# Optimization experiments

Hardware: AMD Instinct MI355X
Metric: run time of the kernel (lower is better)

The kernel has to match this reference:

```python
import jax, jax.numpy as jnp
import numpy as np

B, T, C, H = 4, 2048, 1024, 16
D = C // H  # head dim = 64


def _layernorm(x, g, b, eps=1e-5):
    mu = jnp.mean(x, axis=-1, keepdims=True)
    var = jnp.var(x, axis=-1, keepdims=True)
    return (x - mu) * jax.lax.rsqrt(var + eps) * g + b


def setup_inputs() -> dict:
    key = jax.random.key(0)
    ks = jax.random.split(key, 8)
    s = 0.02
    return {
        "x": jax.random.normal(ks[0], (B, T, C), dtype=jnp.float32),
        "ln1_g": jnp.ones((C,), jnp.float32),
        "ln1_b": jnp.zeros((C,), jnp.float32),
        "W_qkv": jax.random.normal(ks[1], (C, 3 * C), dtype=jnp.float32) * s,
        "b_qkv": jnp.zeros((3 * C,), jnp.float32),
        "W_o": jax.random.normal(ks[2], (C, C), dtype=jnp.float32) * s,
        "b_o": jnp.zeros((C,), jnp.float32),
        "ln2_g": jnp.ones((C,), jnp.float32),
        "ln2_b": jnp.zeros((C,), jnp.float32),
        "W_fc": jax.random.normal(ks[3], (C, 4 * C), dtype=jnp.float32) * s,
        "b_fc": jnp.zeros((4 * C,), jnp.float32),
        "W_pr": jax.random.normal(ks[4], (4 * C, C), dtype=jnp.float32) * s,
        "b_pr": jnp.zeros((C,), jnp.float32),
    }


def reference(x, ln1_g, ln1_b, W_qkv, b_qkv, W_o, b_o, ln2_g, ln2_b, W_fc, b_fc, W_pr, b_pr):
    # --- attention sub-block ---
    h = _layernorm(x, ln1_g, ln1_b)
    qkv = h @ W_qkv + b_qkv                       # [B,T,3C]
    q, k, v = jnp.split(qkv, 3, axis=-1)
    q = q.reshape(B, T, H, D).transpose(0, 2, 1, 3)  # [B,H,T,D]
    k = k.reshape(B, T, H, D).transpose(0, 2, 1, 3)
    v = v.reshape(B, T, H, D).transpose(0, 2, 1, 3)
    att = jnp.einsum("bhqd,bhkd->bhqk", q, k) * (1.0 / jnp.sqrt(jnp.float32(D)))
    causal = jnp.tril(jnp.ones((T, T), dtype=bool))
    att = jnp.where(causal, att, jnp.float32(-jnp.inf))
    att = jax.nn.softmax(att, axis=-1)
    y = jnp.einsum("bhqk,bhkd->bhqd", att, v)     # [B,H,T,D]
    y = y.transpose(0, 2, 1, 3).reshape(B, T, C)
    y = y @ W_o + b_o
    x = x + y
    # --- FFN sub-block ---
    h2 = _layernorm(x, ln2_g, ln2_b)
    f = jax.nn.gelu(h2 @ W_fc + b_fc, approximate=False)  # nn.GELU default = exact
    f = f @ W_pr + b_pr
    return x + f
```

## Files before the change

### kernel.cpp

```cpp
#include <hip/hip_runtime.h>
#include <math.h>

#define Bz 4
#define Tz 2048
#define Cz 1024
#define Hz 16
#define Dz 64
#define MTOK (Bz*Tz)

typedef __attribute__((ext_vector_type(8))) short short8;
typedef __attribute__((ext_vector_type(4))) short short4v;
typedef __attribute__((ext_vector_type(4))) float f32x4;

typedef unsigned int u32_g __attribute__((address_space(1)));
typedef unsigned int u32_l __attribute__((address_space(3)));

__device__ __forceinline__ unsigned short f2bf(float f) {
    unsigned int u = __float_as_uint(f);
    u += 0x7fffu + ((u >> 16) & 1u);
    return (unsigned short)(u >> 16);
}
__device__ __forceinline__ float bf2f(unsigned short h) {
    return __uint_as_float((unsigned int)h << 16);
}

__device__ __forceinline__ void async_cp16(const unsigned short* g, unsigned short* l) {
    __builtin_amdgcn_global_load_lds((const u32_g*)g, (u32_l*)l, 16, 0, 0);
}

__global__ void transpose_w(const float* __restrict__ W, unsigned short* __restrict__ Wt,
                            int K, int N) {
    __shared__ float tile[32][33];
    int n0 = blockIdx.x * 32, k0 = blockIdx.y * 32;
    int tx = threadIdx.x, ty = threadIdx.y;
    #pragma unroll
    for (int i = 0; i < 4; i++)
        tile[ty + i * 8][tx] = W[(size_t)(k0 + ty + i * 8) * N + n0 + tx];
    __syncthreads();
    #pragma unroll
    for (int i = 0; i < 4; i++)
        Wt[(size_t)(n0 + ty + i * 8) * K + k0 + tx] = f2bf(tile[tx][ty + i * 8]);
}

__global__ void ln_kernel(const float* __restrict__ x, const float* __restrict__ g,
                          const float* __restrict__ bb, unsigned short* __restrict__ out) {
    int tok = blockIdx.x, tid = threadIdx.x;
    const float4 v = ((const float4*)(x + (size_t)tok * Cz))[tid];
    float s = v.x + v.y + v.z + v.w;
    float sq = v.x * v.x + v.y * v.y + v.z * v.z + v.w * v.w;
    #pragma unroll
    for (int m = 1; m < 64; m <<= 1) { s += __shfl_xor(s, m); sq += __shfl_xor(sq, m); }
    __shared__ float red[8];
    int lane = tid & 63, wid = tid >> 6;
    if (!lane) { red[wid] = s; red[4 + wid] = sq; }
    __syncthreads();
    s = red[0] + red[1] + red[2] + red[3];
    sq = red[4] + red[5] + red[6] + red[7];
    float mu = s * (1.0f / Cz);
    float var = sq * (1.0f / Cz) - mu * mu;
    float rs = rsqrtf(var + 1e-5f);
    float4 gv = ((const float4*)g)[tid];
    float4 bv = ((const float4*)bb)[tid];
    short4v o;
    o[0] = f2bf((v.x - mu) * rs * gv.x + bv.x);
    o[1] = f2bf((v.y - mu) * rs * gv.y + bv.y);
    o[2] = f2bf((v.z - mu) * rs * gv.z + bv.z);
    o[3] = f2bf((v.w - mu) * rs * gv.w + bv.w);
    *(short4v*)(out + (size_t)tok * Cz + tid * 4) = o;
}

#define MODE_QKV 0
#define MODE_RESID 1
#define MODE_GELU 2

template <int MODE>
__launch_bounds__(256)
__global__ void gemm_bt(const unsigned short* __restrict__ A, const unsigned short* __restrict__ Bt,
                        int ld, int K, int N, const float* __restrict__ bias,
                        float* __restrict__ outf, unsigned short* __restrict__ outb,
                        const float* __restrict__ resid,
                        unsigned short* __restrict__ qo, unsigned short* __restrict__ ko,
                        unsigned short* __restrict__ vo) {
    __shared__ __align__(16) unsigned short As[128 * 64];
    __shared__ __align__(16) unsigned short Bs[128 * 64];
    const int tid = threadIdx.x;
    const int lane = tid & 63;
    const int quad = lane >> 4, l15 = lane & 15;
    const int wid = tid >> 6;
    const int m0 = blockIdx.y * 128, n0 = blockIdx.x * 128;
    const int wm = (wid >> 1) * 64, wn = (wid & 1) * 64;
    f32x4 acc[4][4] = {};

    const int srow = lane >> 3;
    const int scol = ((lane & 7) ^ srow) * 8;
    const unsigned short* Ag[4];
    const unsigned short* Bg[4];
    unsigned short* lA[4];
    unsigned short* lB[4];
    #pragma unroll
    for (int j = 0; j < 4; j++) {
        const int row = wid * 32 + j * 8 + srow;
        Ag[j] = A + (size_t)(m0 + row) * ld + scol;
        Bg[j] = Bt + (size_t)(n0 + row) * ld + scol;
        lA[j] = &As[(wid * 4 + j) * 512 + lane * 8];
        lB[j] = &Bs[(wid * 4 + j) * 512 + lane * 8];
    }

    for (int k0 = 0; k0 < K; k0 += 64) {
        #pragma unroll
        for (int j = 0; j < 4; j++) async_cp16(Ag[j] + k0, lA[j]);
        #pragma unroll
        for (int j = 0; j < 4; j++) async_cp16(Bg[j] + k0, lB[j]);
        __syncthreads();
        #pragma unroll
        for (int ks = 0; ks < 2; ks++) {
            short8 af[4], bfr[4];
            #pragma unroll
            for (int i = 0; i < 4; i++) {
                const int ra = wm + i * 16 + l15;
                af[i] = *(const short8*)&As[ra * 64 + (((ks << 2) + quad) ^ (ra & 7)) * 8];
            }
            #pragma unroll
            for (int i = 0; i < 4; i++) {
                const int rb = wn + i * 16 + l15;
                bfr[i] = *(const short8*)&Bs[rb * 64 + (((ks << 2) + quad) ^ (rb & 7)) * 8];
            }
            #pragma unroll
            for (int mi = 0; mi < 4; mi++)
                #pragma unroll
                for (int ni = 0; ni < 4; ni++)
                    acc[mi][ni] = __builtin_amdgcn_mfma_f32_16x16x32_bf16(af[mi], bfr[ni], acc[mi][ni], 0, 0, 0);
        }
        __syncthreads();
    }

    #pragma unroll
    for (int ni = 0; ni < 4; ni++) {
        const int col = n0 + wn + ni * 16 + l15;
        const float bv = bias[col];
        #pragma unroll
        for (int mi = 0; mi < 4; mi++) {
            #pragma unroll
            for (int r = 0; r < 4; r++) {
                const int row = m0 + wm + mi * 16 + quad * 4 + r;
                float val = acc[mi][ni][r] + bv;
                if constexpr (MODE == MODE_QKV) {
                    int which = col >> 10, cc = col & 1023;
                    int hh = cc >> 6, dd = cc & 63;
                    int b_ = row >> 11, t = row & 2047;
                    if (which == 2) {
                        vo[((size_t)(b_ * Hz + hh) * Dz + dd) * Tz + t] = f2bf(val);
                    } else {
                        unsigned short* dst = which ? ko : qo;
                        dst[((size_t)(b_ * Hz + hh) * Tz + t) * Dz + dd] = f2bf(val);
                    }
                } else if constexpr (MODE == MODE_RESID) {
                    size_t idx = (size_t)row * N + col;
                    outf[idx] = val + resid[idx];
                } else {
                    float c = val * (1.0f + 0.044715f * val * val);
                    float e = __expf(1.5957691216057308f * c);
                    float gz = val * e / (1.0f + e);
                    outb[(size_t)row * N + col] = f2bf(gz);
                }
            }
        }
    }
}

#define ATT_SC 0.18033688011112042f
__launch_bounds__(256)
__global__ void attn_kernel(const unsigned short* __restrict__ qb, const unsigned short* __restrict__ kb,
                            const unsigned short* __restrict__ vt, unsigned short* __restrict__ y) {
    __shared__ __align__(16) unsigned short Klds[64 * 72];
    __shared__ __align__(16) unsigned short Vtl[64 * 72];
    __shared__ __align__(16) unsigned short Plds[4][16 * 72];
    const int tid = threadIdx.x;
    const int lane = tid & 63, wid = tid >> 6;
    const int quad = lane >> 4, l15 = lane & 15;
    const int bh = blockIdx.x & 63;
    const int qt = 15 - (int)(blockIdx.x >> 6);
    const size_t baseT = (size_t)bh * Tz;
    const size_t vbase = (size_t)bh * Dz;
    const int qb0 = qt * 128;

    short8 qf[2][2];
    {
        const unsigned short* q0p = qb + (baseT + qb0 + wid * 16 + l15) * Dz + quad * 8;
        qf[0][0] = *(const short8*)q0p;
        qf[0][1] = *(const short8*)(q0p + 32);
        const unsigned short* q1p = q0p + (size_t)64 * Dz;
        qf[1][0] = *(const short8*)q1p;
        qf[1][1] = *(const short8*)(q1p + 32);
    }

    f32x4 o[2][4] = {};
    float lsum[2][4] = {{0.f,0.f,0.f,0.f},{0.f,0.f,0.f,0.f}};

    const int krow = tid >> 3;
    const int kcol = (tid & 7) * 8;
    const int nchunk = 2 * qt + 2;

    for (int ci = 0; ci < nchunk; ci++) {
        const int k0 = ci * 64;
        *(short8*)&Klds[krow * 72 + kcol]        = *(const short8*)(kb + (baseT + k0 + krow) * Dz + kcol);
        *(short8*)&Klds[(krow + 32) * 72 + kcol] = *(const short8*)(kb + (baseT + k0 + krow + 32) * Dz + kcol);
        *(short8*)&Vtl[krow * 72 + kcol]         = *(const short8*)(vt + (vbase + krow) * Tz + k0 + kcol);
        *(short8*)&Vtl[(krow + 32) * 72 + kcol]  = *(const short8*)(vt + (vbase + krow + 32) * Tz + k0 + kcol);
        __syncthreads();

        #pragma unroll
        for (int t = 0; t < 2; t++) {
            if (t == 0 && ci == nchunk - 1) continue;
            const bool diag = (ci == nchunk - 2 + t);

            f32x4 s[4];
            #pragma unroll
            for (int c = 0; c < 4; c++) {
                short8 kf0 = *(const short8*)&Klds[(c * 16 + l15) * 72 + quad * 8];
                short8 kf1 = *(const short8*)&Klds[(c * 16 + l15) * 72 + 32 + quad * 8];
                f32x4 z = {};
                z = __builtin_amdgcn_mfma_f32_16x16x32_bf16(qf[t][0], kf0, z, 0, 0, 0);
                s[c] = __builtin_amdgcn_mfma_f32_16x16x32_bf16(qf[t][1], kf1, z, 0, 0, 0);
            }
            const int qr = qb0 + t * 64 + wid * 16 + quad * 4;
            #pragma unroll
            for (int c = 0; c < 4; c++)
                #pragma unroll
                for (int r = 0; r < 4; r++) {
                    float p = exp2f(s[c][r] * ATT_SC);
                    if (diag) {
                        int key = k0 + c * 16 + l15;
                        p = (key <= qr + r) ? p : 0.f;
                    }
                    s[c][r] = p;
                    lsum[t][r] += p;
                }
            unsigned short* P = Plds[wid];
            #pragma unroll
            for (int c = 0; c < 4; c++)
                #pragma unroll
                for (int r = 0; r < 4; r++)
                    P[(quad * 4 + r) * 72 + c * 16 + l15] = f2bf(s[c][r]);
            short8 pf0 = *(const short8*)&P[l15 * 72 + quad * 8];
            short8 pf1 = *(const short8*)&P[l15 * 72 + 32 + quad * 8];
            #pragma unroll
            for (int nc = 0; nc < 4; nc++) {
                short8 vf0 = *(const short8*)&Vtl[(nc * 16 + l15) * 72 + quad * 8];
                short8 vf1 = *(const short8*)&Vtl[(nc * 16 + l15) * 72 + 32 + quad * 8];
                o[t][nc] = __builtin_amdgcn_mfma_f32_16x16x32_bf16(pf0, vf0, o[t][nc], 0, 0, 0);
                o[t][nc] = __builtin_amdgcn_mfma_f32_16x16x32_bf16(pf1, vf1, o[t][nc], 0, 0, 0);
            }
        }
        __syncthreads();
    }

    const int b_ = bh >> 4, hh = bh & 15;
    #pragma unroll
    for (int t = 0; t < 2; t++)
        #pragma unroll
        for (int r = 0; r < 4; r++) {
            float ls = lsum[t][r];
            #pragma unroll
            for (int m = 1; m < 16; m <<= 1) ls += __shfl_xor(ls, m);
            float inv = 1.0f / ls;
            size_t tok = (size_t)qb0 + t * 64 + wid * 16 + quad * 4 + r;
            unsigned short* yr = y + ((size_t)b_ * Tz + tok) * Cz + hh * Dz;
            #pragma unroll
            for (int nc = 0; nc < 4; nc++)
                yr[nc * 16 + l15] = f2bf(o[t][nc][r] * inv);
        }
}

extern "C" void kernel_launch(void* const* d_in, const int* in_sizes, int n_in,
                              void* d_out, int out_size, void* d_ws, size_t ws_size,
                              hipStream_t stream) {
    const float* x    = (const float*)d_in[0];
    const float* ln1g = (const float*)d_in[1];
    const float* ln1b = (const float*)d_in[2];
    const float* Wqkv = (const float*)d_in[3];
    const float* bqkv = (const float*)d_in[4];
    const float* Wo   = (const float*)d_in[5];
    const float* bo   = (const float*)d_in[6];
    const float* ln2g = (const float*)d_in[7];
    const float* ln2b = (const float*)d_in[8];
    const float* Wfc  = (const float*)d_in[9];
    const float* bfc  = (const float*)d_in[10];
    const float* Wpr  = (const float*)d_in[11];
    const float* bpr  = (const float*)d_in[12];
    float* out = (float*)d_out;

    char* ws = (char*)d_ws;
    size_t off = 0;
    auto alloc = [&](size_t bytes) { void* p = ws + off; off += (bytes + 255) & ~(size_t)255; return p; };
    unsigned short* wqkv_t = (unsigned short*)alloc((size_t)3072 * 1024 * 2);
    unsigned short* wo_t   = (unsigned short*)alloc((size_t)1024 * 1024 * 2);
    unsigned short* wfc_t  = (unsigned short*)alloc((size_t)4096 * 1024 * 2);
    unsigned short* wpr_t  = (unsigned short*)alloc((size_t)1024 * 4096 * 2);
    unsigned short* h1     = (unsigned short*)alloc((size_t)MTOK * Cz * 2);
    unsigned short* qbuf   = (unsigned short*)alloc((size_t)MTOK * Cz * 2);
    unsigned short* kbuf   = (unsigned short*)alloc((size_t)MTOK * Cz * 2);
    unsigned short* vbuf   = (unsigned short*)alloc((size_t)MTOK * Cz * 2);
    unsigned short* ybuf   = (unsigned short*)alloc((size_t)MTOK * Cz * 2);
    float*          x1     = (float*)alloc((size_t)MTOK * Cz * 4);
    unsigned short* h2     = (unsigned short*)alloc((size_t)MTOK * Cz * 2);
    unsigned short* fbuf   = (unsigned short*)alloc((size_t)MTOK * 4096 * 2);

    dim3 tb(32, 8);
    transpose_w<<<dim3(3072 / 32, 1024 / 32), tb, 0, stream>>>(Wqkv, wqkv_t, 1024, 3072);
    transpose_w<<<dim3(1024 / 32, 1024 / 32), tb, 0, stream>>>(Wo, wo_t, 1024, 1024);
    transpose_w<<<dim3(4096 / 32, 1024 / 32), tb, 0, stream>>>(Wfc, wfc_t, 1024, 4096);
    transpose_w<<<dim3(1024 / 32, 4096 / 32), tb, 0, stream>>>(Wpr, wpr_t, 4096, 1024);

    ln_kernel<<<MTOK, 256, 0, stream>>>(x, ln1g, ln1b, h1);
    gemm_bt<MODE_QKV><<<dim3(24, 64), 256, 0, stream>>>(h1, wqkv_t, 1024, 1024, 3072, bqkv,
                                                        nullptr, nullptr, nullptr, qbuf, kbuf, vbuf);
    attn_kernel<<<1024, 256, 0, stream>>>(qbuf, kbuf, vbuf, ybuf);
    gemm_bt<MODE_RESID><<<dim3(8, 64), 256, 0, stream>>>(ybuf, wo_t, 1024, 1024, 1024, bo,
                                                         x1, nullptr, x, nullptr, nullptr, nullptr);
    ln_kernel<<<MTOK, 256, 0, stream>>>(x1, ln2g, ln2b, h2);
    gemm_bt<MODE_GELU><<<dim3(32, 64), 256, 0, stream>>>(h2, wfc_t, 1024, 1024, 4096, bfc,
                                                         nullptr, fbuf, nullptr, nullptr, nullptr, nullptr);
    gemm_bt<MODE_RESID><<<dim3(8, 64), 256, 0, stream>>>(fbuf, wpr_t, 4096, 4096, 1024, bpr,
                                                         out, nullptr, x1, nullptr, nullptr, nullptr);
}
```

Baseline: 589.2 us.

## Remap GEMM blocks for XCD-aware L2 reuse and async-load attention K/V tiles

The GEMM grid becomes 1D. Block IDs are remapped so that blocks landing on the same XCD (id mod 8) share B-column tiles and consecutive M rows, which should improve L2 locality across the 8 chiplets. The attention kernel now loads K and V^T tiles with async global-to-LDS copies into an unpadded, XOR-swizzled 64x64 layout instead of going through registers into padded LDS, with reads adjusted to match the swizzle. This cuts register traffic and LDS footprint, but depends on the async-copy helper and swizzle being correct.

```diff
diff --git a/kernel.cpp b/kernel.cpp
--- a/kernel.cpp
+++ b/kernel.cpp
@@ -87,7 +87,9 @@
     const int lane = tid & 63;
     const int quad = lane >> 4, l15 = lane & 15;
     const int wid = tid >> 6;
-    const int m0 = blockIdx.y * 128, n0 = blockIdx.x * 128;
+    const int id = blockIdx.x;
+    const int m0 = ((id & 7) * 8 + ((id >> 3) & 7)) * 128;
+    const int n0 = (id >> 6) * 128;
     const int wm = (wid >> 1) * 64, wn = (wid & 1) * 64;
     f32x4 acc[4][4] = {};
 
@@ -172,8 +174,8 @@
 __launch_bounds__(256)
 __global__ void attn_kernel(const unsigned short* __restrict__ qb, const unsigned short* __restrict__ kb,
                             const unsigned short* __restrict__ vt, unsigned short* __restrict__ y) {
-    __shared__ __align__(16) unsigned short Klds[64 * 72];
-    __shared__ __align__(16) unsigned short Vtl[64 * 72];
+    __shared__ __align__(16) unsigned short Klds[64 * 64];
+    __shared__ __align__(16) unsigned short Vtl[64 * 64];
     __shared__ __align__(16) unsigned short Plds[4][16 * 72];
     const int tid = threadIdx.x;
     const int lane = tid & 63, wid = tid >> 6;
@@ -197,16 +199,25 @@
     f32x4 o[2][4] = {};
     float lsum[2][4] = {{0.f,0.f,0.f,0.f},{0.f,0.f,0.f,0.f}};
 
-    const int krow = tid >> 3;
-    const int kcol = (tid & 7) * 8;
+    const int srow = lane >> 3;
+    const int swz = ((lane & 7) ^ srow) * 8;
+    const unsigned short* kg0 = kb + (baseT + wid * 8 + srow) * Dz + swz;
+    const unsigned short* kg1 = kg0 + (size_t)32 * Dz;
+    const unsigned short* vg0 = vt + (vbase + wid * 8 + srow) * Tz + swz;
+    const unsigned short* vg1 = vg0 + (size_t)32 * Tz;
+    unsigned short* kl0 = &Klds[wid * 512 + lane * 8];
+    unsigned short* kl1 = kl0 + 2048;
+    unsigned short* vl0 = &Vtl[wid * 512 + lane * 8];
+    unsigned short* vl1 = vl0 + 2048;
+
     const int nchunk = 2 * qt + 2;
 
     for (int ci = 0; ci < nchunk; ci++) {
         const int k0 = ci * 64;
-        *(short8*)&Klds[krow * 72 + kcol]        = *(const short8*)(kb + (baseT + k0 + krow) * Dz + kcol);
-        *(short8*)&Klds[(krow + 32) * 72 + kcol] = *(const short8*)(kb + (baseT + k0 + krow + 32) * Dz + kcol);
-        *(short8*)&Vtl[krow * 72 + kcol]         = *(const short8*)(vt + (vbase + krow) * Tz + k0 + kcol);
-        *(short8*)&Vtl[(krow + 32) * 72 + kcol]  = *(const short8*)(vt + (vbase + krow + 32) * Tz + k0 + kcol);
+        async_cp16(kg0 + (size_t)k0 * Dz, kl0);
+        async_cp16(kg1 + (size_t)k0 * Dz, kl1);
+        async_cp16(vg0 + k0, vl0);
+        async_cp16(vg1 + k0, vl1);
         __syncthreads();
 
         #pragma unroll
@@ -217,8 +228,9 @@
             f32x4 s[4];
             #pragma unroll
             for (int c = 0; c < 4; c++) {
-                short8 kf0 = *(const short8*)&Klds[(c * 16 + l15) * 72 + quad * 8];
-                short8 kf1 = *(const short8*)&Klds[(c * 16 + l15) * 72 + 32 + quad * 8];
+                const int rk = c * 16 + l15;
+                short8 kf0 = *(const short8*)&Klds[rk * 64 + ((quad ^ (rk & 7)) * 8)];
+                short8 kf1 = *(const short8*)&Klds[rk * 64 + (((quad + 4) ^ (rk & 7)) * 8)];
                 f32x4 z = {};
                 z = __builtin_amdgcn_mfma_f32_16x16x32_bf16(qf[t][0], kf0, z, 0, 0, 0);
                 s[c] = __builtin_amdgcn_mfma_f32_16x16x32_bf16(qf[t][1], kf1, z, 0, 0, 0);
@@ -246,8 +258,9 @@
             short8 pf1 = *(const short8*)&P[l15 * 72 + 32 + quad * 8];
             #pragma unroll
             for (int nc = 0; nc < 4; nc++) {
-                short8 vf0 = *(const short8*)&Vtl[(nc * 16 + l15) * 72 + quad * 8];
-                short8 vf1 = *(const short8*)&Vtl[(nc * 16 + l15) * 72 + 32 + quad * 8];
+                const int rv = nc * 16 + l15;
+                short8 vf0 = *(const short8*)&Vtl[rv * 64 + ((quad ^ (rv & 7)) * 8)];
+                short8 vf1 = *(const short8*)&Vtl[rv * 64 + (((quad + 4) ^ (rv & 7)) * 8)];
                 o[t][nc] = __builtin_amdgcn_mfma_f32_16x16x32_bf16(pf0, vf0, o[t][nc], 0, 0, 0);
                 o[t][nc] = __builtin_amdgcn_mfma_f32_16x16x32_bf16(pf1, vf1, o[t][nc], 0, 0, 0);
             }
@@ -313,14 +326,14 @@
     transpose_w<<<dim3(1024 / 32, 4096 / 32), tb, 0, stream>>>(Wpr, wpr_t, 4096, 1024);
 
     ln_kernel<<<MTOK, 256, 0, stream>>>(x, ln1g, ln1b, h1);
-    gemm_bt<MODE_QKV><<<dim3(24, 64), 256, 0, stream>>>(h1, wqkv_t, 1024, 1024, 3072, bqkv,
-                                                        nullptr, nullptr, nullptr, qbuf, kbuf, vbuf);
+    gemm_bt<MODE_QKV><<<64 * 24, 256, 0, stream>>>(h1, wqkv_t, 1024, 1024, 3072, bqkv,
+                                                   nullptr, nullptr, nullptr, qbuf, kbuf, vbuf);
     attn_kernel<<<1024, 256, 0, stream>>>(qbuf, kbuf, vbuf, ybuf);
-    gemm_bt<MODE_RESID><<<dim3(8, 64), 256, 0, stream>>>(ybuf, wo_t, 1024, 1024, 1024, bo,
-                                                         x1, nullptr, x, nullptr, nullptr, nullptr);
+    gemm_bt<MODE_RESID><<<64 * 8, 256, 0, stream>>>(ybuf, wo_t, 1024, 1024, 1024, bo,
+                                                    x1, nullptr, x, nullptr, nullptr, nullptr);
     ln_kernel<<<MTOK, 256, 0, stream>>>(x1, ln2g, ln2b, h2);
-    gemm_bt<MODE_GELU><<<dim3(32, 64), 256, 0, stream>>>(h2, wfc_t, 1024, 1024, 4096, bfc,
-                                                         nullptr, fbuf, nullptr, nullptr, nullptr, nullptr);
-    gemm_bt<MODE_RESID><<<dim3(8, 64), 256, 0, stream>>>(fbuf, wpr_t, 4096, 4096, 1024, bpr,
-                                                         out, nullptr, x1, nullptr, nullptr, nullptr);
-}
+    gemm_bt<MODE_GELU><<<64 * 32, 256, 0, stream>>>(h2, wfc_t, 1024, 1024, 4096, bfc,
+                                                    nullptr, fbuf, nullptr, nullptr, nullptr, nullptr);
+    gemm_bt<MODE_RESID><<<64 * 8, 256, 0, stream>>>(fbuf, wpr_t, 4096, 4096, 1024, bpr,
+                                                    out, nullptr, x1, nullptr, nullptr, nullptr);
+}
```

New measurement: 528.4 us. 10.3% less time.
